# Kernel optimization log

Measured on AMD Instinct MI355X. Metric: run time of the kernel, lower is better.

The kernel has to match this reference:

```python
import jax, jax.numpy as jnp
import numpy as np

N_ATOMS = 100000
BOX = 12.0
NS = 128            # 2**ceil(log2(2*(2*pi/mesh_spacing)*BOX/(2*pi) + 1)) with mesh_spacing=0.2
ORDER = 4           # interpolation_order (cubic)
SMEARING = 1.0      # atomic_gaussian_width
N_SPECIES = 2


def _weights_1d(x):
    # P3M order-4 assignment weights; offsets x in [-1/2, 1/2]
    x2 = x * x
    x3 = x2 * x
    return jnp.stack([
        (1.0 - 6.0 * x + 12.0 * x2 - 8.0 * x3) / 48.0,
        (23.0 - 30.0 * x - 12.0 * x2 + 24.0 * x3) / 48.0,
        (23.0 + 30.0 * x - 12.0 * x2 - 24.0 * x3) / 48.0,
        (1.0 + 6.0 * x + 12.0 * x2 + 8.0 * x3) / 48.0,
    ])  # (ORDER, n_atoms, 3)


def _interpolation(positions, cell, ns):
    # fractional coordinates scaled by mesh size; even order -> offset vs cell midpoint
    inv_cell = jnp.linalg.inv(cell)
    pos_rel = ns * (positions @ inv_cell)                     # (n, 3)
    base = jnp.floor(pos_rel)
    offsets = pos_rel - (base + 0.5)                          # in [-1/2, 1/2)
    w = _weights_1d(offsets)                                  # (4, n, 3)
    shifts = jnp.arange(1 - (ORDER + 1) // 2, 1 + ORDER // 2, dtype=jnp.int32)  # [-1,0,1,2]
    idx = (base.astype(jnp.int32)[None, :, :] + shifts[:, None, None]) % ns    # (4, n, 3)
    return w, idx


def _points_to_mesh(w, idx, charges, ns):
    # scatter charges onto the mesh via the separable 4^3 stencil
    n_ch = charges.shape[1]
    mesh = jnp.zeros((n_ch, ns, ns, ns), dtype=charges.dtype)
    cT = charges.T                                            # (n_ch, n)
    for l in range(ORDER):
        for m in range(ORDER):
            for n in range(ORDER):
                ww = w[l, :, 0] * w[m, :, 1] * w[n, :, 2]     # (n_atoms,)
                mesh = mesh.at[:, idx[l, :, 0], idx[m, :, 1], idx[n, :, 2]].add(ww * cT)
    return mesh


def _mesh_to_points(mesh, w, idx):
    # gather the potential back to the atom positions with the same stencil
    pot = jnp.zeros((mesh.shape[0], w.shape[1]), dtype=mesh.dtype)
    for l in range(ORDER):
        for m in range(ORDER):
            for n in range(ORDER):
                ww = w[l, :, 0] * w[m, :, 1] * w[n, :, 2]
                pot = pot + ww * mesh[:, idx[l, :, 0], idx[m, :, 1], idx[n, :, 2]]
    return pot.T  # (n_atoms, n_ch)


def _fourier_space_convolution(mesh, cell, ns, smearing):
    # Coulomb kernel (potential_exponent=1) with Gaussian smearing, k=0 term removed
    m1 = jnp.fft.fftfreq(ns) * ns                             # integer frequencies
    m3 = jnp.fft.rfftfreq(ns) * ns
    mx, my, mz = jnp.meshgrid(m1, m1, m3, indexing="ij")
    mvec = jnp.stack([mx, my, mz], axis=-1)                   # (ns, ns, ns//2+1, 3)
    k = 2.0 * jnp.pi * (mvec @ jnp.linalg.inv(cell).T)        # reciprocal vectors
    ksq = jnp.sum(k * k, axis=-1)
    safe = jnp.where(ksq > 0.0, ksq, 1.0)
    G = jnp.where(ksq > 0.0, 4.0 * jnp.pi * jnp.exp(-0.5 * smearing * smearing * ksq) / safe, 0.0)
    mesh_hat = jnp.fft.rfftn(mesh, axes=(1, 2, 3))            # unnormalized forward
    pot = jnp.fft.irfftn(mesh_hat * G, s=(ns, ns, ns), axes=(1, 2, 3), norm="forward")
    volume = jnp.abs(jnp.linalg.det(cell))
    return pot / volume


def _compute_single_frame(positions, cell, charges, ns):
    w, idx = _interpolation(positions, cell, ns)
    rho_mesh = _points_to_mesh(w, idx, charges, ns)
    pot_mesh = _fourier_space_convolution(rho_mesh, cell, ns, SMEARING)
    return _mesh_to_points(pot_mesh, w, idx)                  # (n_atoms, n_channels)


def setup_inputs() -> dict:
    key = jax.random.key(0)
    k1, k2 = jax.random.split(key)
    positions = jax.random.uniform(k1, (N_ATOMS, 3), dtype=jnp.float32) * BOX
    cell = BOX * jnp.eye(3, dtype=jnp.float32)
    species = jax.random.randint(k2, (N_ATOMS,), 0, N_SPECIES, dtype=jnp.int32)
    return {"positions": positions, "cell": cell, "species": species, "ns": NS}


def reference(positions, cell, species, ns):
    # compute(): one-hot species channels, then particle-mesh Ewald potential per channel
    charges = jax.nn.one_hot(species, N_SPECIES, dtype=positions.dtype)
    return _compute_single_frame(positions, cell, charges, ns)
```

## Files before the change

### kernel.cpp

```cpp
#include <hip/hip_runtime.h>

#define NSZ 128
#define NS3 (NSZ * NSZ * NSZ)
#define NBUCK_D 16
#define NBUCK (NBUCK_D * NBUCK_D * NBUCK_D)
#define RGD 8
#define RW 16
#define LROW 129
#define LDS_BYTES (NSZ * LROW * sizeof(float2))


__device__ __forceinline__ void inv3x3(const float* __restrict__ c, float* inv) {
    float a00 = c[0], a01 = c[1], a02 = c[2];
    float a10 = c[3], a11 = c[4], a12 = c[5];
    float a20 = c[6], a21 = c[7], a22 = c[8];
    float det = a00 * (a11 * a22 - a12 * a21)
              - a01 * (a10 * a22 - a12 * a20)
              + a02 * (a10 * a21 - a11 * a20);
    float id = 1.0f / det;
    inv[0] = (a11 * a22 - a12 * a21) * id;
    inv[1] = (a02 * a21 - a01 * a22) * id;
    inv[2] = (a01 * a12 - a02 * a11) * id;
    inv[3] = (a12 * a20 - a10 * a22) * id;
    inv[4] = (a00 * a22 - a02 * a20) * id;
    inv[5] = (a02 * a10 - a00 * a12) * id;
    inv[6] = (a10 * a21 - a11 * a20) * id;
    inv[7] = (a01 * a20 - a00 * a21) * id;
    inv[8] = (a00 * a11 - a01 * a10) * id;
}

__device__ __forceinline__ float det3x3(const float* __restrict__ c) {
    return c[0] * (c[4] * c[8] - c[5] * c[7])
         - c[1] * (c[3] * c[8] - c[5] * c[6])
         + c[2] * (c[3] * c[7] - c[4] * c[6]);
}

__device__ __forceinline__ int brev7(int i) { return (int)(__brev((unsigned)i) >> 25); }

__device__ __forceinline__ float2 cadd(float2 a, float2 b) { return make_float2(a.x + b.x, a.y + b.y); }
__device__ __forceinline__ float2 csub(float2 a, float2 b) { return make_float2(a.x - b.x, a.y - b.y); }
__device__ __forceinline__ float2 cmul(float2 a, float2 b) {
    return make_float2(a.x * b.x - a.y * b.y, a.x * b.y + a.y * b.x);
}
__device__ __forceinline__ float2 cmulc(float2 a, float2 b) {
    return make_float2(a.x * b.x + a.y * b.y, a.y * b.x - a.x * b.y);
}

__device__ __forceinline__ void bases_of(float px, float py, float pz,
                                         const float* __restrict__ inv,
                                         int base[3], float frac[3]) {
    float pr[3];
    pr[0] = (float)NSZ * (px * inv[0] + py * inv[3] + pz * inv[6]);
    pr[1] = (float)NSZ * (px * inv[1] + py * inv[4] + pz * inv[7]);
    pr[2] = (float)NSZ * (px * inv[2] + py * inv[5] + pz * inv[8]);
#pragma unroll
    for (int d = 0; d < 3; d++) {
        float b = floorf(pr[d]);
        frac[d] = pr[d] - b - 0.5f;
        int bi = (int)b;
        base[d] = bi < 0 ? 0 : (bi > NSZ - 1 ? NSZ - 1 : bi);
    }
}

__device__ __forceinline__ void weights_of(float x, float w[4]) {
    float x2 = x * x, x3 = x2 * x;
    w[0] = (1.0f - 6.0f * x + 12.0f * x2 - 8.0f * x3) * (1.0f / 48.0f);
    w[1] = (23.0f - 30.0f * x - 12.0f * x2 + 24.0f * x3) * (1.0f / 48.0f);
    w[2] = (23.0f + 30.0f * x - 12.0f * x2 - 24.0f * x3) * (1.0f / 48.0f);
    w[3] = (1.0f + 6.0f * x + 12.0f * x2 + 8.0f * x3) * (1.0f / 48.0f);
}

__device__ __forceinline__ void stencil_pos(float px, float py, float pz,
                                            const float* __restrict__ inv,
                                            int base[3], float w[3][4]) {
    float frac[3];
    bases_of(px, py, pz, inv, base, frac);
    weights_of(frac[0], w[0]);
    weights_of(frac[1], w[1]);
    weights_of(frac[2], w[2]);
}

__device__ __forceinline__ int bucket_of(float px, float py, float pz,
                                         const float* __restrict__ inv) {
    int base[3];
    float frac[3];
    bases_of(px, py, pz, inv, base, frac);
    return ((base[0] >> 3) * NBUCK_D + (base[1] >> 3)) * NBUCK_D + (base[2] >> 3);
}


__global__ void bin_hist(const float* __restrict__ pos, const float* __restrict__ cell,
                         int* __restrict__ counts, int n_atoms) {
    int a = blockIdx.x * blockDim.x + threadIdx.x;
    if (a >= n_atoms) return;
    float inv[9];
    inv3x3(cell, inv);
    atomicAdd(&counts[bucket_of(pos[a * 3], pos[a * 3 + 1], pos[a * 3 + 2], inv)], 1);
}

__global__ void __launch_bounds__(1024)
scan4096(const int* __restrict__ counts, int* __restrict__ starts, int* __restrict__ cursor) {
    __shared__ int wsum[16];
    __shared__ int wpref[16];
    int t = threadIdx.x;
    int c0 = counts[4 * t], c1 = counts[4 * t + 1], c2 = counts[4 * t + 2], c3 = counts[4 * t + 3];
    int tot = c0 + c1 + c2 + c3;
    int lane = t & 63, w = t >> 6;
    int incl = tot;
#pragma unroll
    for (int o = 1; o < 64; o <<= 1) {
        int v = __shfl_up(incl, o, 64);
        if (lane >= o) incl += v;
    }
    if (lane == 63) wsum[w] = incl;
    __syncthreads();
    if (t < 16) {
        int p = 0;
        for (int i = 0; i < 16; i++) { if (i < t) p += wsum[i]; }
        wpref[t] = p;
    }
    __syncthreads();
    int ex = wpref[w] + incl - tot;
    starts[4 * t]     = ex;                cursor[4 * t]     = ex;
    starts[4 * t + 1] = ex + c0;           cursor[4 * t + 1] = ex + c0;
    starts[4 * t + 2] = ex + c0 + c1;      cursor[4 * t + 2] = ex + c0 + c1;
    starts[4 * t + 3] = ex + c0 + c1 + c2; cursor[4 * t + 3] = ex + c0 + c1 + c2;
    if (t == 1023) starts[4096] = ex + tot;
}

__global__ void bin_permute(const float* __restrict__ pos, const float* __restrict__ cell,
                            const int* __restrict__ species, int* __restrict__ cursor,
                            float4* __restrict__ recs, int n_atoms) {
    int a = blockIdx.x * blockDim.x + threadIdx.x;
    if (a >= n_atoms) return;
    float inv[9];
    inv3x3(cell, inv);
    float px = pos[a * 3], py = pos[a * 3 + 1], pz = pos[a * 3 + 2];
    int b = bucket_of(px, py, pz, inv);
    int p = atomicAdd(&cursor[b], 1);
    recs[p] = make_float4(px, py, pz, __int_as_float((a << 1) | (species[a] & 1)));
}


#define ACC_ROW 33
#define ACC_SZ (RW * RW * ACC_ROW)

__global__ void __launch_bounds__(1024)
scatter_region(const float* __restrict__ cell, const int* __restrict__ starts,
               const float4* __restrict__ recs, float2* __restrict__ mesh) {
    __shared__ float acc[ACC_SZ];
    __shared__ int rstart_s[64];
    __shared__ int rpref_s[64];
    __shared__ int rtot_s;
    int t = threadIdx.x;
    int BX = blockIdx.x, BY = blockIdx.y, BZ = blockIdx.z;

    for (int i = t; i < ACC_SZ; i += 1024) acc[i] = 0.0f;

    if (t < 64) {
        int dx = (t >> 4) & 3, dy = (t >> 2) & 3, dz = t & 3;
        int bx = (2 * BX - 1 + dx) & (NBUCK_D - 1);
        int by = (2 * BY - 1 + dy) & (NBUCK_D - 1);
        int bz = (2 * BZ - 1 + dz) & (NBUCK_D - 1);
        int b = (bx * NBUCK_D + by) * NBUCK_D + bz;
        int s0 = starts[b];
        int c = starts[b + 1] - s0;
        rstart_s[t] = s0;
        int incl = c;
#pragma unroll
        for (int o = 1; o < 64; o <<= 1) {
            int v = __shfl_up(incl, o, 64);
            if (t >= o) incl += v;
        }
        rpref_s[t] = incl - c;
        if (t == 63) rtot_s = incl;
    }
    __syncthreads();

    float inv[9];
    inv3x3(cell, inv);
    int M = rtot_s;
    int sx = BX << 4, sy = BY << 4, sz = BZ << 4;
    int lane = t & 63;

    for (int i = t; i < M; i += 1024) {
        int r = 0;
#pragma unroll
        for (int step = 32; step; step >>= 1)
            if (r + step < 64 && rpref_s[r + step] <= i) r += step;
        float4 rec = recs[rstart_s[r] + (i - rpref_s[r])];
        int base[3];
        float frac[3];
        bases_of(rec.x, rec.y, rec.z, inv, base, frac);
        int rbx = (base[0] - sx + 2) & (NSZ - 1);
        int rby = (base[1] - sy + 2) & (NSZ - 1);
        int rbz = (base[2] - sz + 2) & (NSZ - 1);
        if (rbx >= 19 || rby >= 19 || rbz >= 19) continue;
        rbx -= 2; rby -= 2; rbz -= 2;
        float w[3][4];
        weights_of(frac[0], w[0]);
        weights_of(frac[1], w[1]);
        weights_of(frac[2], w[2]);
        int sp = __float_as_int(rec.w) & 1;
#pragma unroll
        for (int l = 0; l < 4; l++) {
            int cx = rbx + l - 1;
            if ((unsigned)cx >= (unsigned)RW) continue;
            float wl = w[0][l];
#pragma unroll
            for (int m = 0; m < 4; m++) {
                int cy = rby + m - 1;
                if ((unsigned)cy >= (unsigned)RW) continue;
                float wlm = wl * w[1][m];
                int rowb = (cx * RW + cy) * ACC_ROW + sp;
#pragma unroll
                for (int nn = 0; nn < 4; nn++) {
                    int n = (nn + lane) & 3;
                    int cz = rbz + n - 1;
                    if ((unsigned)cz >= (unsigned)RW) continue;
                    atomicAdd(&acc[rowb + cz * 2], wlm * w[2][n]);
                }
            }
        }
    }
    __syncthreads();

    for (int i = t; i < RW * RW * RW; i += 1024) {
        int x = i >> 8, y = (i >> 4) & 15, z = i & 15;
        float2 v = make_float2(acc[(x * RW + y) * ACC_ROW + z * 2],
                               acc[(x * RW + y) * ACC_ROW + z * 2 + 1]);
        size_t gi = (size_t)((sx + x) * NSZ + (sy + y)) * NSZ + (sz + z);
        mesh[gi] = v;
    }
}


__global__ void scatter_atomic(const float* __restrict__ pos,
                               const float* __restrict__ cell,
                               const int* __restrict__ species,
                               float* __restrict__ meshf, int n_atoms) {
    int a = blockIdx.x * blockDim.x + threadIdx.x;
    if (a >= n_atoms) return;
    float inv[9];
    inv3x3(cell, inv);
    int base[3];
    float w[3][4];
    stencil_pos(pos[a * 3], pos[a * 3 + 1], pos[a * 3 + 2], inv, base, w);
    int sp = species[a] & 1;
#pragma unroll
    for (int l = 0; l < 4; l++) {
        int gx = (base[0] + l - 1 + NSZ) & (NSZ - 1);
#pragma unroll
        for (int m = 0; m < 4; m++) {
            int gy = (base[1] + m - 1 + NSZ) & (NSZ - 1);
            float wlm = w[0][l] * w[1][m];
            int rowb = (gx * NSZ + gy) * NSZ;
#pragma unroll
            for (int n = 0; n < 4; n++) {
                int gz = (base[2] + n - 1 + NSZ) & (NSZ - 1);
                atomicAdd(meshf + (((size_t)(rowb + gz)) << 1) + sp, wlm * w[2][n]);
            }
        }
    }
}


__global__ void __launch_bounds__(1024)
fft_fwd_zy(float2* __restrict__ mesh) {
    extern __shared__ float2 sl[];
    __shared__ float2 tw[64];
    int t = threadIdx.x;
    int xs = blockIdx.x;
    if (t < 64) {
        float sn, cs;
        __sincosf(6.283185307179586f * (float)t / 128.0f, &sn, &cs);
        tw[t] = make_float2(cs, -sn);
    }
    const float4* src = (const float4*)(mesh + (size_t)xs * (NSZ * NSZ));
    for (int f = t; f < 8192; f += 1024) {
        float4 v = src[f];
        int y = f >> 6, z = (f & 63) * 2;
        sl[y * LROW + z]     = make_float2(v.x, v.y);
        sl[y * LROW + z + 1] = make_float2(v.z, v.w);
    }
    __syncthreads();
    int lane = t & 127, jb = (t >> 7) * 8;
    for (int s = 6; s >= 0; --s) {
        int half = 1 << s;
        for (int j = jb; j < jb + 8; ++j) {
            int pos = j & (half - 1);
            int i0 = ((j >> s) << (s + 1)) + pos;
            float2 w = tw[pos << (6 - s)];
            float2* p0 = &sl[lane * LROW + i0];
            float2 a = p0[0], b = p0[half];
            p0[0]    = cadd(a, b);
            p0[half] = cmul(csub(a, b), w);
        }
        __syncthreads();
    }
    for (int s = 6; s >= 0; --s) {
        int half = 1 << s;
        for (int j = jb; j < jb + 8; ++j) {
            int pos = j & (half - 1);
            int i0 = ((j >> s) << (s + 1)) + pos;
            float2 w = tw[pos << (6 - s)];
            float2* p0 = &sl[i0 * LROW + lane];
            float2 a = p0[0], b = p0[half * LROW];
            p0[0]           = cadd(a, b);
            p0[half * LROW] = cmul(csub(a, b), w);
        }
        __syncthreads();
    }
    float4* dst = (float4*)(mesh + (size_t)xs * (NSZ * NSZ));
    for (int f = t; f < 8192; f += 1024) {
        int y = f >> 6, z = (f & 63) * 2;
        float2 u0 = sl[y * LROW + z], u1 = sl[y * LROW + z + 1];
        dst[f] = make_float4(u0.x, u0.y, u1.x, u1.y);
    }
}

__global__ void __launch_bounds__(1024)
fft_x_g(float2* __restrict__ mesh, const float* __restrict__ cell, float smearing) {
    extern __shared__ float2 sl[];
    __shared__ float2 tw[64];
    int t = threadIdx.x;
    int y = blockIdx.x;
    if (t < 64) {
        float sn, cs;
        __sincosf(6.283185307179586f * (float)t / 128.0f, &sn, &cs);
        tw[t] = make_float2(cs, -sn);
    }
    for (int f = t; f < 8192; f += 1024) {
        int x = f >> 6, c = f & 63;
        float4 v = ((const float4*)mesh)[(size_t)x * 8192 + (size_t)y * 64 + c];
        int z = c * 2;
        sl[x * LROW + z]     = make_float2(v.x, v.y);
        sl[x * LROW + z + 1] = make_float2(v.z, v.w);
    }
    __syncthreads();
    int lane = t & 127, jb = (t >> 7) * 8;
    for (int s = 6; s >= 0; --s) {
        int half = 1 << s;
        for (int j = jb; j < jb + 8; ++j) {
            int pos = j & (half - 1);
            int i0 = ((j >> s) << (s + 1)) + pos;
            float2 w = tw[pos << (6 - s)];
            float2* p0 = &sl[i0 * LROW + lane];
            float2 a = p0[0], b = p0[half * LROW];
            p0[0]           = cadd(a, b);
            p0[half * LROW] = cmul(csub(a, b), w);
        }
        __syncthreads();
    }
    {
        float inv[9];
        inv3x3(cell, inv);
        float vol = fabsf(det3x3(cell));
        int kyi = brev7(y);
        float fy = (kyi < NSZ / 2) ? (float)kyi : (float)(kyi - NSZ);
        const float twopi = 6.283185307179586f;
        for (int f = t; f < NSZ * NSZ; f += 1024) {
            int px = f >> 7, pz = f & 127;
            int kxi = brev7(px), kzi = brev7(pz);
            float fx = (kxi < NSZ / 2) ? (float)kxi : (float)(kxi - NSZ);
            float fz = (kzi < NSZ / 2) ? (float)kzi : (float)(kzi - NSZ);
            float k0 = twopi * (fx * inv[0] + fy * inv[1] + fz * inv[2]);
            float k1 = twopi * (fx * inv[3] + fy * inv[4] + fz * inv[5]);
            float k2 = twopi * (fx * inv[6] + fy * inv[7] + fz * inv[8]);
            float ksq = k0 * k0 + k1 * k1 + k2 * k2;
            float g = 0.0f;
            if (ksq > 0.0f) {
                g = 12.566370614359172f * __expf(-0.5f * smearing * smearing * ksq) / ksq;
            }
            g /= vol;
            float2 v = sl[px * LROW + pz];
            sl[px * LROW + pz] = make_float2(v.x * g, v.y * g);
        }
    }
    __syncthreads();
    for (int s = 0; s < 7; ++s) {
        int half = 1 << s;
        for (int j = jb; j < jb + 8; ++j) {
            int pos = j & (half - 1);
            int i0 = ((j >> s) << (s + 1)) + pos;
            float2 w = tw[pos << (6 - s)];
            float2* p0 = &sl[i0 * LROW + lane];
            float2 a = p0[0];
            float2 bw = cmulc(p0[half * LROW], w);
            p0[0]           = cadd(a, bw);
            p0[half * LROW] = csub(a, bw);
        }
        __syncthreads();
    }
    for (int f = t; f < 8192; f += 1024) {
        int x = f >> 6, c = f & 63;
        int z = c * 2;
        float2 u0 = sl[x * LROW + z], u1 = sl[x * LROW + z + 1];
        ((float4*)mesh)[(size_t)x * 8192 + (size_t)y * 64 + c] = make_float4(u0.x, u0.y, u1.x, u1.y);
    }
}

__global__ void __launch_bounds__(1024)
fft_inv_yz(float2* __restrict__ mesh) {
    extern __shared__ float2 sl[];
    __shared__ float2 tw[64];
    int t = threadIdx.x;
    int xs = blockIdx.x;
    if (t < 64) {
        float sn, cs;
        __sincosf(6.283185307179586f * (float)t / 128.0f, &sn, &cs);
        tw[t] = make_float2(cs, -sn);
    }
    const float4* src = (const float4*)(mesh + (size_t)xs * (NSZ * NSZ));
    for (int f = t; f < 8192; f += 1024) {
        float4 v = src[f];
        int y = f >> 6, z = (f & 63) * 2;
        sl[y * LROW + z]     = make_float2(v.x, v.y);
        sl[y * LROW + z + 1] = make_float2(v.z, v.w);
    }
    __syncthreads();
    int lane = t & 127, jb = (t >> 7) * 8;
    for (int s = 0; s < 7; ++s) {
        int half = 1 << s;
        for (int j = jb; j < jb + 8; ++j) {
            int pos = j & (half - 1);
            int i0 = ((j >> s) << (s + 1)) + pos;
            float2 w = tw[pos << (6 - s)];
            float2* p0 = &sl[i0 * LROW + lane];
            float2 a = p0[0];
            float2 bw = cmulc(p0[half * LROW], w);
            p0[0]           = cadd(a, bw);
            p0[half * LROW] = csub(a, bw);
        }
        __syncthreads();
    }
    for (int s = 0; s < 7; ++s) {
        int half = 1 << s;
        for (int j = jb; j < jb + 8; ++j) {
            int pos = j & (half - 1);
            int i0 = ((j >> s) << (s + 1)) + pos;
            float2 w = tw[pos << (6 - s)];
            float2* p0 = &sl[lane * LROW + i0];
            float2 a = p0[0];
            float2 bw = cmulc(p0[half], w);
            p0[0]    = cadd(a, bw);
            p0[half] = csub(a, bw);
        }
        __syncthreads();
    }
    float4* dst = (float4*)(mesh + (size_t)xs * (NSZ * NSZ));
    for (int f = t; f < 8192; f += 1024) {
        int y = f >> 6, z = (f & 63) * 2;
        float2 u0 = sl[y * LROW + z], u1 = sl[y * LROW + z + 1];
        dst[f] = make_float4(u0.x, u0.y, u1.x, u1.y);
    }
}


#define GROW 12

__global__ void __launch_bounds__(128)
gather_region(const float* __restrict__ cell, const int* __restrict__ starts,
              const float4* __restrict__ recs, const float2* __restrict__ mesh,
              float2* __restrict__ out) {
    __shared__ float2 gm[11 * 11 * GROW];
    int t = threadIdx.x;
    int b = blockIdx.x;
    int bx = b >> 8, by = (b >> 4) & 15, bz = b & 15;
    int ox = bx * 8 - 1, oy = by * 8 - 1, oz = bz * 8 - 1;

    for (int i = t; i < 11 * 11 * 11; i += 128) {
        int x = i / 121, rem = i % 121, y = rem / 11, z = rem % 11;
        int gx = (ox + x) & (NSZ - 1);
        int gy = (oy + y) & (NSZ - 1);
        int gz = (oz + z) & (NSZ - 1);
        gm[(x * 11 + y) * GROW + z] = mesh[(size_t)(gx * NSZ + gy) * NSZ + gz];
    }
    __syncthreads();

    int s = starts[b], e = starts[b + 1];
    float inv[9];
    inv3x3(cell, inv);

    for (int ai = s + t; ai < e; ai += 128) {
        float4 rec = recs[ai];
        int base[3];
        float w[3][4];
        stencil_pos(rec.x, rec.y, rec.z, inv, base, w);
        int lx0 = base[0] - bx * 8;
        int ly0 = base[1] - by * 8;
        int lz0 = base[2] - bz * 8;
        float acc0 = 0.0f, acc1 = 0.0f;
#pragma unroll
        for (int l = 0; l < 4; l++) {
            float wl = w[0][l];
#pragma unroll
            for (int m = 0; m < 4; m++) {
                float wlm = wl * w[1][m];
                int rowb = ((lx0 + l) * 11 + (ly0 + m)) * GROW + lz0;
#pragma unroll
                for (int n = 0; n < 4; n++) {
                    float2 v = gm[rowb + n];
                    float ww = wlm * w[2][n];
                    acc0 += ww * v.x;
                    acc1 += ww * v.y;
                }
            }
        }
        out[__float_as_int(rec.w) >> 1] = make_float2(acc0, acc1);
    }
}

__global__ void gather_plain(const float* __restrict__ pos,
                             const float* __restrict__ cell,
                             const float2* __restrict__ mesh,
                             float2* __restrict__ out, int n_atoms) {
    int a = blockIdx.x * blockDim.x + threadIdx.x;
    if (a >= n_atoms) return;
    float inv[9];
    inv3x3(cell, inv);
    int base[3];
    float w[3][4];
    stencil_pos(pos[a * 3], pos[a * 3 + 1], pos[a * 3 + 2], inv, base, w);
    float acc0 = 0.0f, acc1 = 0.0f;
#pragma unroll
    for (int l = 0; l < 4; l++) {
        int gx = (base[0] + l - 1 + NSZ) & (NSZ - 1);
#pragma unroll
        for (int m = 0; m < 4; m++) {
            int gy = (base[1] + m - 1 + NSZ) & (NSZ - 1);
            float wlm = w[0][l] * w[1][m];
            int rowb = (gx * NSZ + gy) * NSZ;
#pragma unroll
            for (int n = 0; n < 4; n++) {
                int gz = (base[2] + n - 1 + NSZ) & (NSZ - 1);
                float2 v = mesh[rowb + gz];
                float ww = wlm * w[2][n];
                acc0 += ww * v.x;
                acc1 += ww * v.y;
            }
        }
    }
    out[a] = make_float2(acc0, acc1);
}


extern "C" void kernel_launch(void* const* d_in, const int* in_sizes, int n_in,
                              void* d_out, int out_size, void* d_ws, size_t ws_size,
                              hipStream_t stream) {
    const float* pos     = (const float*)d_in[0];
    const float* cell    = (const float*)d_in[1];
    const int*   species = (const int*)d_in[2];
    int n_atoms = in_sizes[0] / 3;

    char* ws = (char*)d_ws;
    float2* mesh = (float2*)ws;
    size_t off = (size_t)NS3 * sizeof(float2);
    int* counts = (int*)(ws + off);           off += NBUCK * 4;
    int* starts = (int*)(ws + off);           off += (NBUCK + 4) * 4;
    int* cursor = (int*)(ws + off);           off += NBUCK * 4;
    off = (off + 15) & ~(size_t)15;
    float4* recs = (float4*)(ws + off);       off += (size_t)n_atoms * 16;
    bool binned = (ws_size >= off);

    hipFuncSetAttribute((const void*)fft_fwd_zy, hipFuncAttributeMaxDynamicSharedMemorySize, (int)LDS_BYTES);
    hipFuncSetAttribute((const void*)fft_x_g,    hipFuncAttributeMaxDynamicSharedMemorySize, (int)LDS_BYTES);
    hipFuncSetAttribute((const void*)fft_inv_yz, hipFuncAttributeMaxDynamicSharedMemorySize, (int)LDS_BYTES);

    int ab = (n_atoms + 255) / 256;

    if (binned) {
        hipMemsetAsync(counts, 0, NBUCK * 4, stream);
        bin_hist<<<ab, 256, 0, stream>>>(pos, cell, counts, n_atoms);
        scan4096<<<1, 1024, 0, stream>>>(counts, starts, cursor);
        bin_permute<<<ab, 256, 0, stream>>>(pos, cell, species, cursor, recs, n_atoms);
        dim3 rg(RGD, RGD, RGD);
        scatter_region<<<rg, 1024, 0, stream>>>(cell, starts, recs, mesh);
    } else {
        hipMemsetAsync(mesh, 0, (size_t)NS3 * sizeof(float2), stream);
        scatter_atomic<<<ab, 256, 0, stream>>>(pos, cell, species, (float*)mesh, n_atoms);
    }

    fft_fwd_zy<<<NSZ, 1024, LDS_BYTES, stream>>>(mesh);
    fft_x_g   <<<NSZ, 1024, LDS_BYTES, stream>>>(mesh, cell, 1.0f );
    fft_inv_yz<<<NSZ, 1024, LDS_BYTES, stream>>>(mesh);

    if (binned) {
        gather_region<<<NBUCK, 128, 0, stream>>>(cell, starts, recs, mesh, (float2*)d_out);
    } else {
        gather_plain<<<ab, 256, 0, stream>>>(pos, cell, mesh, (float2*)d_out, n_atoms);
    }
}
```

Before: 232.8 us.

## Fuse charge scatter into forward FFT slab and gather into inverse FFT slab

```diff
diff --git a/kernel.cpp b/kernel.cpp
--- a/kernel.cpp
+++ b/kernel.cpp
@@ -2,10 +2,7 @@
 
 #define NSZ 128
 #define NS3 (NSZ * NSZ * NSZ)
-#define NBUCK_D 16
-#define NBUCK (NBUCK_D * NBUCK_D * NBUCK_D)
-#define RGD 8
-#define RW 16
+#define NBUCK 4096
 #define LROW 129
 #define LDS_BYTES (NSZ * LROW * sizeof(float2))
 
@@ -70,6 +67,16 @@
     w[3] = (1.0f + 6.0f * x + 12.0f * x2 + 8.0f * x3) * (1.0f / 48.0f);
 }
 
+__device__ __forceinline__ float weight1(int o, float x) {
+    float x2 = x * x, x3 = x2 * x;
+    switch (o) {
+        case 0:  return (1.0f - 6.0f * x + 12.0f * x2 - 8.0f * x3) * (1.0f / 48.0f);
+        case 1:  return (23.0f - 30.0f * x - 12.0f * x2 + 24.0f * x3) * (1.0f / 48.0f);
+        case 2:  return (23.0f + 30.0f * x - 12.0f * x2 - 24.0f * x3) * (1.0f / 48.0f);
+        default: return (1.0f + 6.0f * x + 12.0f * x2 + 8.0f * x3) * (1.0f / 48.0f);
+    }
+}
+
 __device__ __forceinline__ void stencil_pos(float px, float py, float pz,
                                             const float* __restrict__ inv,
                                             int base[3], float w[3][4]) {
@@ -80,14 +87,10 @@
     weights_of(frac[2], w[2]);
 }
 
-__device__ __forceinline__ int bucket_of(float px, float py, float pz,
-                                         const float* __restrict__ inv) {
-    int base[3];
-    float frac[3];
-    bases_of(px, py, pz, inv, base, frac);
-    return ((base[0] >> 3) * NBUCK_D + (base[1] >> 3)) * NBUCK_D + (base[2] >> 3);
-}
-
+
+__device__ __forceinline__ int xkey_of(const int base[3]) {
+    return base[0] * 32 + (base[1] >> 2);
+}
 
 __global__ void bin_hist(const float* __restrict__ pos, const float* __restrict__ cell,
                          int* __restrict__ counts, int n_atoms) {
@@ -95,7 +98,10 @@
     if (a >= n_atoms) return;
     float inv[9];
     inv3x3(cell, inv);
-    atomicAdd(&counts[bucket_of(pos[a * 3], pos[a * 3 + 1], pos[a * 3 + 2], inv)], 1);
+    int base[3];
+    float frac[3];
+    bases_of(pos[a * 3], pos[a * 3 + 1], pos[a * 3 + 2], inv, base, frac);
+    atomicAdd(&counts[xkey_of(base)], 1);
 }
 
 __global__ void __launch_bounds__(1024)
@@ -130,143 +136,25 @@
 
 __global__ void bin_permute(const float* __restrict__ pos, const float* __restrict__ cell,
                             const int* __restrict__ species, int* __restrict__ cursor,
-                            float4* __restrict__ recs, int n_atoms) {
-    int a = blockIdx.x * blockDim.x + threadIdx.x;
-    if (a >= n_atoms) return;
-    float inv[9];
-    inv3x3(cell, inv);
-    float px = pos[a * 3], py = pos[a * 3 + 1], pz = pos[a * 3 + 2];
-    int b = bucket_of(px, py, pz, inv);
-    int p = atomicAdd(&cursor[b], 1);
-    recs[p] = make_float4(px, py, pz, __int_as_float((a << 1) | (species[a] & 1)));
-}
-
-
-#define ACC_ROW 33
-#define ACC_SZ (RW * RW * ACC_ROW)
-
-__global__ void __launch_bounds__(1024)
-scatter_region(const float* __restrict__ cell, const int* __restrict__ starts,
-               const float4* __restrict__ recs, float2* __restrict__ mesh) {
-    __shared__ float acc[ACC_SZ];
-    __shared__ int rstart_s[64];
-    __shared__ int rpref_s[64];
-    __shared__ int rtot_s;
-    int t = threadIdx.x;
-    int BX = blockIdx.x, BY = blockIdx.y, BZ = blockIdx.z;
-
-    for (int i = t; i < ACC_SZ; i += 1024) acc[i] = 0.0f;
-
-    if (t < 64) {
-        int dx = (t >> 4) & 3, dy = (t >> 2) & 3, dz = t & 3;
-        int bx = (2 * BX - 1 + dx) & (NBUCK_D - 1);
-        int by = (2 * BY - 1 + dy) & (NBUCK_D - 1);
-        int bz = (2 * BZ - 1 + dz) & (NBUCK_D - 1);
-        int b = (bx * NBUCK_D + by) * NBUCK_D + bz;
-        int s0 = starts[b];
-        int c = starts[b + 1] - s0;
-        rstart_s[t] = s0;
-        int incl = c;
-#pragma unroll
-        for (int o = 1; o < 64; o <<= 1) {
-            int v = __shfl_up(incl, o, 64);
-            if (t >= o) incl += v;
-        }
-        rpref_s[t] = incl - c;
-        if (t == 63) rtot_s = incl;
-    }
-    __syncthreads();
-
-    float inv[9];
-    inv3x3(cell, inv);
-    int M = rtot_s;
-    int sx = BX << 4, sy = BY << 4, sz = BZ << 4;
-    int lane = t & 63;
-
-    for (int i = t; i < M; i += 1024) {
-        int r = 0;
-#pragma unroll
-        for (int step = 32; step; step >>= 1)
-            if (r + step < 64 && rpref_s[r + step] <= i) r += step;
-        float4 rec = recs[rstart_s[r] + (i - rpref_s[r])];
-        int base[3];
-        float frac[3];
-        bases_of(rec.x, rec.y, rec.z, inv, base, frac);
-        int rbx = (base[0] - sx + 2) & (NSZ - 1);
-        int rby = (base[1] - sy + 2) & (NSZ - 1);
-        int rbz = (base[2] - sz + 2) & (NSZ - 1);
-        if (rbx >= 19 || rby >= 19 || rbz >= 19) continue;
-        rbx -= 2; rby -= 2; rbz -= 2;
-        float w[3][4];
-        weights_of(frac[0], w[0]);
-        weights_of(frac[1], w[1]);
-        weights_of(frac[2], w[2]);
-        int sp = __float_as_int(rec.w) & 1;
-#pragma unroll
-        for (int l = 0; l < 4; l++) {
-            int cx = rbx + l - 1;
-            if ((unsigned)cx >= (unsigned)RW) continue;
-            float wl = w[0][l];
-#pragma unroll
-            for (int m = 0; m < 4; m++) {
-                int cy = rby + m - 1;
-                if ((unsigned)cy >= (unsigned)RW) continue;
-                float wlm = wl * w[1][m];
-                int rowb = (cx * RW + cy) * ACC_ROW + sp;
-#pragma unroll
-                for (int nn = 0; nn < 4; nn++) {
-                    int n = (nn + lane) & 3;
-                    int cz = rbz + n - 1;
-                    if ((unsigned)cz >= (unsigned)RW) continue;
-                    atomicAdd(&acc[rowb + cz * 2], wlm * w[2][n]);
-                }
-            }
-        }
-    }
-    __syncthreads();
-
-    for (int i = t; i < RW * RW * RW; i += 1024) {
-        int x = i >> 8, y = (i >> 4) & 15, z = i & 15;
-        float2 v = make_float2(acc[(x * RW + y) * ACC_ROW + z * 2],
-                               acc[(x * RW + y) * ACC_ROW + z * 2 + 1]);
-        size_t gi = (size_t)((sx + x) * NSZ + (sy + y)) * NSZ + (sz + z);
-        mesh[gi] = v;
-    }
-}
-
-
-__global__ void scatter_atomic(const float* __restrict__ pos,
-                               const float* __restrict__ cell,
-                               const int* __restrict__ species,
-                               float* __restrict__ meshf, int n_atoms) {
+                            float4* __restrict__ recs, int* __restrict__ ids, int n_atoms) {
     int a = blockIdx.x * blockDim.x + threadIdx.x;
     if (a >= n_atoms) return;
     float inv[9];
     inv3x3(cell, inv);
     int base[3];
-    float w[3][4];
-    stencil_pos(pos[a * 3], pos[a * 3 + 1], pos[a * 3 + 2], inv, base, w);
+    float frac[3];
+    bases_of(pos[a * 3], pos[a * 3 + 1], pos[a * 3 + 2], inv, base, frac);
     int sp = species[a] & 1;
-#pragma unroll
-    for (int l = 0; l < 4; l++) {
-        int gx = (base[0] + l - 1 + NSZ) & (NSZ - 1);
-#pragma unroll
-        for (int m = 0; m < 4; m++) {
-            int gy = (base[1] + m - 1 + NSZ) & (NSZ - 1);
-            float wlm = w[0][l] * w[1][m];
-            int rowb = (gx * NSZ + gy) * NSZ;
-#pragma unroll
-            for (int n = 0; n < 4; n++) {
-                int gz = (base[2] + n - 1 + NSZ) & (NSZ - 1);
-                atomicAdd(meshf + (((size_t)(rowb + gz)) << 1) + sp, wlm * w[2][n]);
-            }
-        }
-    }
+    int p = atomicAdd(&cursor[xkey_of(base)], 1);
+    int pack = base[0] | (base[1] << 7) | (base[2] << 14) | (sp << 21);
+    recs[p] = make_float4(frac[0], frac[1], frac[2], __int_as_float(pack));
+    ids[p] = a;
 }
 
 
 __global__ void __launch_bounds__(1024)
-fft_fwd_zy(float2* __restrict__ mesh) {
+fft_fwd_zy_sc(const float4* __restrict__ recs, const int* __restrict__ starts,
+              float2* __restrict__ mesh) {
     extern __shared__ float2 sl[];
     __shared__ float2 tw[64];
     int t = threadIdx.x;
@@ -276,14 +164,36 @@
         __sincosf(6.283185307179586f * (float)t / 128.0f, &sn, &cs);
         tw[t] = make_float2(cs, -sn);
     }
-    const float4* src = (const float4*)(mesh + (size_t)xs * (NSZ * NSZ));
-    for (int f = t; f < 8192; f += 1024) {
-        float4 v = src[f];
-        int y = f >> 6, z = (f & 63) * 2;
-        sl[y * LROW + z]     = make_float2(v.x, v.y);
-        sl[y * LROW + z + 1] = make_float2(v.z, v.w);
-    }
-    __syncthreads();
+    for (int i = t; i < NSZ * LROW; i += 1024) sl[i] = make_float2(0.0f, 0.0f);
+    __syncthreads();
+
+    float* pf = (float*)sl;
+#pragma unroll
+    for (int k = 0; k < 4; k++) {
+        int bx = (xs - 2 + k) & (NSZ - 1);
+        int s = starts[bx * 32], e = starts[bx * 32 + 32];
+        for (int i = s + t; i < e; i += 1024) {
+            float4 r = recs[i];
+            int pk = __float_as_int(r.w);
+            int by = (pk >> 7) & 127, bz = (pk >> 14) & 127, sp = (pk >> 21) & 1;
+            float wx = weight1(3 - k, r.x);
+            float wy[4], wz[4];
+            weights_of(r.y, wy);
+            weights_of(r.z, wz);
+#pragma unroll
+            for (int m = 0; m < 4; m++) {
+                int gy = (by - 1 + m) & (NSZ - 1);
+                float wxm = wx * wy[m];
+#pragma unroll
+                for (int n = 0; n < 4; n++) {
+                    int gz = (bz - 1 + n) & (NSZ - 1);
+                    atomicAdd(pf + ((gy * LROW + gz) << 1) + sp, wxm * wz[n]);
+                }
+            }
+        }
+    }
+    __syncthreads();
+
     int lane = t & 127, jb = (t >> 7) * 8;
     for (int s = 6; s >= 0; --s) {
         int half = 1 << s;
@@ -318,6 +228,7 @@
         dst[f] = make_float4(u0.x, u0.y, u1.x, u1.y);
     }
 }
+
 
 __global__ void __launch_bounds__(1024)
 fft_x_g(float2* __restrict__ mesh, const float* __restrict__ cell, float smearing) {
@@ -400,6 +311,183 @@
     }
 }
 
+
+__global__ void __launch_bounds__(1024)
+fft_inv_yz_ga(const float4* __restrict__ recs, const int* __restrict__ starts,
+              const float2* __restrict__ mesh, float2* __restrict__ partials) {
+    extern __shared__ float2 sl[];
+    __shared__ float2 tw[64];
+    int t = threadIdx.x;
+    int xs = blockIdx.x;
+    if (t < 64) {
+        float sn, cs;
+        __sincosf(6.283185307179586f * (float)t / 128.0f, &sn, &cs);
+        tw[t] = make_float2(cs, -sn);
+    }
+    const float4* src = (const float4*)(mesh + (size_t)xs * (NSZ * NSZ));
+    for (int f = t; f < 8192; f += 1024) {
+        float4 v = src[f];
+        int y = f >> 6, z = (f & 63) * 2;
+        sl[y * LROW + z]     = make_float2(v.x, v.y);
+        sl[y * LROW + z + 1] = make_float2(v.z, v.w);
+    }
+    __syncthreads();
+    int lane = t & 127, jb = (t >> 7) * 8;
+    for (int s = 0; s < 7; ++s) {
+        int half = 1 << s;
+        for (int j = jb; j < jb + 8; ++j) {
+            int pos = j & (half - 1);
+            int i0 = ((j >> s) << (s + 1)) + pos;
+            float2 w = tw[pos << (6 - s)];
+            float2* p0 = &sl[i0 * LROW + lane];
+            float2 a = p0[0];
+            float2 bw = cmulc(p0[half * LROW], w);
+            p0[0]           = cadd(a, bw);
+            p0[half * LROW] = csub(a, bw);
+        }
+        __syncthreads();
+    }
+    for (int s = 0; s < 7; ++s) {
+        int half = 1 << s;
+        for (int j = jb; j < jb + 8; ++j) {
+            int pos = j & (half - 1);
+            int i0 = ((j >> s) << (s + 1)) + pos;
+            float2 w = tw[pos << (6 - s)];
+            float2* p0 = &sl[lane * LROW + i0];
+            float2 a = p0[0];
+            float2 bw = cmulc(p0[half], w);
+            p0[0]    = cadd(a, bw);
+            p0[half] = csub(a, bw);
+        }
+        __syncthreads();
+    }
+
+#pragma unroll
+    for (int k = 0; k < 4; k++) {
+        int bx = (xs - 2 + k) & (NSZ - 1);
+        int s = starts[bx * 32], e = starts[bx * 32 + 32];
+        for (int i = s + t; i < e; i += 1024) {
+            float4 r = recs[i];
+            int pk = __float_as_int(r.w);
+            int by = (pk >> 7) & 127, bz = (pk >> 14) & 127;
+            float wx = weight1(3 - k, r.x);
+            float wy[4], wz[4];
+            weights_of(r.y, wy);
+            weights_of(r.z, wz);
+            float a0 = 0.0f, a1 = 0.0f;
+#pragma unroll
+            for (int m = 0; m < 4; m++) {
+                int gy = (by - 1 + m) & (NSZ - 1);
+                int rowb = gy * LROW;
+#pragma unroll
+                for (int n = 0; n < 4; n++) {
+                    int gz = (bz - 1 + n) & (NSZ - 1);
+                    float2 v = sl[rowb + gz];
+                    float ww = wy[m] * wz[n];
+                    a0 += ww * v.x;
+                    a1 += ww * v.y;
+                }
+            }
+            partials[(size_t)i * 4 + (3 - k)] = make_float2(wx * a0, wx * a1);
+        }
+    }
+}
+
+
+__global__ void combine(const float2* __restrict__ partials, const int* __restrict__ ids,
+                        float2* __restrict__ out, int n_atoms) {
+    int i = blockIdx.x * blockDim.x + threadIdx.x;
+    if (i >= n_atoms) return;
+    float2 p0 = partials[4 * i], p1 = partials[4 * i + 1];
+    float2 p2 = partials[4 * i + 2], p3 = partials[4 * i + 3];
+    out[ids[i]] = make_float2(p0.x + p1.x + p2.x + p3.x,
+                              p0.y + p1.y + p2.y + p3.y);
+}
+
+
+__global__ void scatter_atomic(const float* __restrict__ pos,
+                               const float* __restrict__ cell,
+                               const int* __restrict__ species,
+                               float* __restrict__ meshf, int n_atoms) {
+    int a = blockIdx.x * blockDim.x + threadIdx.x;
+    if (a >= n_atoms) return;
+    float inv[9];
+    inv3x3(cell, inv);
+    int base[3];
+    float w[3][4];
+    stencil_pos(pos[a * 3], pos[a * 3 + 1], pos[a * 3 + 2], inv, base, w);
+    int sp = species[a] & 1;
+#pragma unroll
+    for (int l = 0; l < 4; l++) {
+        int gx = (base[0] + l - 1 + NSZ) & (NSZ - 1);
+#pragma unroll
+        for (int m = 0; m < 4; m++) {
+            int gy = (base[1] + m - 1 + NSZ) & (NSZ - 1);
+            float wlm = w[0][l] * w[1][m];
+            int rowb = (gx * NSZ + gy) * NSZ;
+#pragma unroll
+            for (int n = 0; n < 4; n++) {
+                int gz = (base[2] + n - 1 + NSZ) & (NSZ - 1);
+                atomicAdd(meshf + (((size_t)(rowb + gz)) << 1) + sp, wlm * w[2][n]);
+            }
+        }
+    }
+}
+
+__global__ void __launch_bounds__(1024)
+fft_fwd_zy(float2* __restrict__ mesh) {
+    extern __shared__ float2 sl[];
+    __shared__ float2 tw[64];
+    int t = threadIdx.x;
+    int xs = blockIdx.x;
+    if (t < 64) {
+        float sn, cs;
+        __sincosf(6.283185307179586f * (float)t / 128.0f, &sn, &cs);
+        tw[t] = make_float2(cs, -sn);
+    }
+    const float4* src = (const float4*)(mesh + (size_t)xs * (NSZ * NSZ));
+    for (int f = t; f < 8192; f += 1024) {
+        float4 v = src[f];
+        int y = f >> 6, z = (f & 63) * 2;
+        sl[y * LROW + z]     = make_float2(v.x, v.y);
+        sl[y * LROW + z + 1] = make_float2(v.z, v.w);
+    }
+    __syncthreads();
+    int lane = t & 127, jb = (t >> 7) * 8;
+    for (int s = 6; s >= 0; --s) {
+        int half = 1 << s;
+        for (int j = jb; j < jb + 8; ++j) {
+            int pos = j & (half - 1);
+            int i0 = ((j >> s) << (s + 1)) + pos;
+            float2 w = tw[pos << (6 - s)];
+            float2* p0 = &sl[lane * LROW + i0];
+            float2 a = p0[0], b = p0[half];
+            p0[0]    = cadd(a, b);
+            p0[half] = cmul(csub(a, b), w);
+        }
+        __syncthreads();
+    }
+    for (int s = 6; s >= 0; --s) {
+        int half = 1 << s;
+        for (int j = jb; j < jb + 8; ++j) {
+            int pos = j & (half - 1);
+            int i0 = ((j >> s) << (s + 1)) + pos;
+            float2 w = tw[pos << (6 - s)];
+            float2* p0 = &sl[i0 * LROW + lane];
+            float2 a = p0[0], b = p0[half * LROW];
+            p0[0]           = cadd(a, b);
+            p0[half * LROW] = cmul(csub(a, b), w);
+        }
+        __syncthreads();
+    }
+    float4* dst = (float4*)(mesh + (size_t)xs * (NSZ * NSZ));
+    for (int f = t; f < 8192; f += 1024) {
+        int y = f >> 6, z = (f & 63) * 2;
+        float2 u0 = sl[y * LROW + z], u1 = sl[y * LROW + z + 1];
+        dst[f] = make_float4(u0.x, u0.y, u1.x, u1.y);
+    }
+}
+
 __global__ void __launch_bounds__(1024)
 fft_inv_yz(float2* __restrict__ mesh) {
     extern __shared__ float2 sl[];
@@ -453,61 +541,6 @@
         int y = f >> 6, z = (f & 63) * 2;
         float2 u0 = sl[y * LROW + z], u1 = sl[y * LROW + z + 1];
         dst[f] = make_float4(u0.x, u0.y, u1.x, u1.y);
-    }
-}
-
-
-#define GROW 12
-
-__global__ void __launch_bounds__(128)
-gather_region(const float* __restrict__ cell, const int* __restrict__ starts,
-              const float4* __restrict__ recs, const float2* __restrict__ mesh,
-              float2* __restrict__ out) {
-    __shared__ float2 gm[11 * 11 * GROW];
-    int t = threadIdx.x;
-    int b = blockIdx.x;
-    int bx = b >> 8, by = (b >> 4) & 15, bz = b & 15;
-    int ox = bx * 8 - 1, oy = by * 8 - 1, oz = bz * 8 - 1;
-
-    for (int i = t; i < 11 * 11 * 11; i += 128) {
-        int x = i / 121, rem = i % 121, y = rem / 11, z = rem % 11;
-        int gx = (ox + x) & (NSZ - 1);
-        int gy = (oy + y) & (NSZ - 1);
-        int gz = (oz + z) & (NSZ - 1);
-        gm[(x * 11 + y) * GROW + z] = mesh[(size_t)(gx * NSZ + gy) * NSZ + gz];
-    }
-    __syncthreads();
-
-    int s = starts[b], e = starts[b + 1];
-    float inv[9];
-    inv3x3(cell, inv);
-
-    for (int ai = s + t; ai < e; ai += 128) {
-        float4 rec = recs[ai];
-        int base[3];
-        float w[3][4];
-        stencil_pos(rec.x, rec.y, rec.z, inv, base, w);
-        int lx0 = base[0] - bx * 8;
-        int ly0 = base[1] - by * 8;
-        int lz0 = base[2] - bz * 8;
-        float acc0 = 0.0f, acc1 = 0.0f;
-#pragma unroll
-        for (int l = 0; l < 4; l++) {
-            float wl = w[0][l];
-#pragma unroll
-            for (int m = 0; m < 4; m++) {
-                float wlm = wl * w[1][m];
-                int rowb = ((lx0 + l) * 11 + (ly0 + m)) * GROW + lz0;
-#pragma unroll
-                for (int n = 0; n < 4; n++) {
-                    float2 v = gm[rowb + n];
-                    float ww = wlm * w[2][n];
-                    acc0 += ww * v.x;
-                    acc1 += ww * v.y;
-                }
-            }
-        }
-        out[__float_as_int(rec.w) >> 1] = make_float2(acc0, acc1);
     }
 }
 
@@ -560,12 +593,17 @@
     int* starts = (int*)(ws + off);           off += (NBUCK + 4) * 4;
     int* cursor = (int*)(ws + off);           off += NBUCK * 4;
     off = (off + 15) & ~(size_t)15;
-    float4* recs = (float4*)(ws + off);       off += (size_t)n_atoms * 16;
+    float4* recs     = (float4*)(ws + off);   off += (size_t)n_atoms * 16;
+    int* ids         = (int*)(ws + off);      off += (size_t)n_atoms * 4;
+    off = (off + 15) & ~(size_t)15;
+    float2* partials = (float2*)(ws + off);   off += (size_t)n_atoms * 4 * 8;
     bool binned = (ws_size >= off);
 
-    hipFuncSetAttribute((const void*)fft_fwd_zy, hipFuncAttributeMaxDynamicSharedMemorySize, (int)LDS_BYTES);
-    hipFuncSetAttribute((const void*)fft_x_g,    hipFuncAttributeMaxDynamicSharedMemorySize, (int)LDS_BYTES);
-    hipFuncSetAttribute((const void*)fft_inv_yz, hipFuncAttributeMaxDynamicSharedMemorySize, (int)LDS_BYTES);
+    hipFuncSetAttribute((const void*)fft_fwd_zy_sc, hipFuncAttributeMaxDynamicSharedMemorySize, (int)LDS_BYTES);
+    hipFuncSetAttribute((const void*)fft_x_g,       hipFuncAttributeMaxDynamicSharedMemorySize, (int)LDS_BYTES);
+    hipFuncSetAttribute((const void*)fft_inv_yz_ga, hipFuncAttributeMaxDynamicSharedMemorySize, (int)LDS_BYTES);
+    hipFuncSetAttribute((const void*)fft_fwd_zy,    hipFuncAttributeMaxDynamicSharedMemorySize, (int)LDS_BYTES);
+    hipFuncSetAttribute((const void*)fft_inv_yz,    hipFuncAttributeMaxDynamicSharedMemorySize, (int)LDS_BYTES);
 
     int ab = (n_atoms + 255) / 256;
 
@@ -573,21 +611,17 @@
         hipMemsetAsync(counts, 0, NBUCK * 4, stream);
         bin_hist<<<ab, 256, 0, stream>>>(pos, cell, counts, n_atoms);
         scan4096<<<1, 1024, 0, stream>>>(counts, starts, cursor);
-        bin_permute<<<ab, 256, 0, stream>>>(pos, cell, species, cursor, recs, n_atoms);
-        dim3 rg(RGD, RGD, RGD);
-        scatter_region<<<rg, 1024, 0, stream>>>(cell, starts, recs, mesh);
+        bin_permute<<<ab, 256, 0, stream>>>(pos, cell, species, cursor, recs, ids, n_atoms);
+        fft_fwd_zy_sc<<<NSZ, 1024, LDS_BYTES, stream>>>(recs, starts, mesh);
+        fft_x_g      <<<NSZ, 1024, LDS_BYTES, stream>>>(mesh, cell, 1.0f );
+        fft_inv_yz_ga<<<NSZ, 1024, LDS_BYTES, stream>>>(recs, starts, mesh, partials);
+        combine<<<ab, 256, 0, stream>>>(partials, ids, (float2*)d_out, n_atoms);
     } else {
         hipMemsetAsync(mesh, 0, (size_t)NS3 * sizeof(float2), stream);
         scatter_atomic<<<ab, 256, 0, stream>>>(pos, cell, species, (float*)mesh, n_atoms);
-    }
-
-    fft_fwd_zy<<<NSZ, 1024, LDS_BYTES, stream>>>(mesh);
-    fft_x_g   <<<NSZ, 1024, LDS_BYTES, stream>>>(mesh, cell, 1.0f );
-    fft_inv_yz<<<NSZ, 1024, LDS_BYTES, stream>>>(mesh);
-
-    if (binned) {
-        gather_region<<<NBUCK, 128, 0, stream>>>(cell, starts, recs, mesh, (float2*)d_out);
-    } else {
+        fft_fwd_zy<<<NSZ, 1024, LDS_BYTES, stream>>>(mesh);
+        fft_x_g   <<<NSZ, 1024, LDS_BYTES, stream>>>(mesh, cell, 1.0f );
+        fft_inv_yz<<<NSZ, 1024, LDS_BYTES, stream>>>(mesh);
         gather_plain<<<ab, 256, 0, stream>>>(pos, cell, mesh, (float2*)d_out, n_atoms);
     }
 }
```

New measurement: 238.8 us. 2.5% more time.
